# Kernel tuning notes

Measured on AMD Instinct MI355X. Metric: run time of the kernel, lower is better.

The kernel has to match this reference:

```python
import jax, jax.numpy as jnp
import numpy as np

N = 2_000_000
C_IN = 32
C_OUT = 64
K_TAPS = 8  # kernel_size=2 in 3D -> 2^3 taps
EPS = 1e-5


def setup_inputs() -> dict:
    key = jax.random.key(0)
    k1, k2, k3, k4, k5 = jax.random.split(key, 5)
    features = jax.random.normal(k1, (N, C_IN), dtype=jnp.float32)
    gamma = jax.random.uniform(k2, (C_IN,), dtype=jnp.float32)
    beta = jnp.zeros((C_IN,), dtype=jnp.float32)
    weight = jax.random.normal(k3, (K_TAPS, C_IN, C_OUT), dtype=jnp.float32)
    # kernel-map: output segment id and kernel-tap id per input point
    out_index = jax.random.randint(k4, (N,), 0, N, dtype=jnp.int64)
    offset_index = jax.random.randint(k5, (N,), 0, K_TAPS, dtype=jnp.int64)
    return {
        "features": features,
        "gamma": gamma,
        "beta": beta,
        "weight": weight,
        "out_index": out_index,
        "offset_index": offset_index,
    }


def reference(features, gamma, beta, weight, out_index, offset_index):
    # BatchNorm over all active points (training-mode batch stats, biased var)
    mean = jnp.mean(features, axis=0)
    var = jnp.var(features, axis=0)
    x = (features - mean) * jax.lax.rsqrt(var + EPS) * gamma + beta
    # ReLU
    x = jnp.maximum(x, 0.0)
    # Sparse conv, stride == kernel_size: each point hits one output cell via one tap.
    # Loop over the fixed 8 kernel taps; mask, dense matmul, scatter-add.
    out = jnp.zeros((N, C_OUT), dtype=features.dtype)
    for tap in range(K_TAPS):
        xt = jnp.where((offset_index == tap)[:, None], x, 0.0)  # [N, C_in]
        contrib = xt @ weight[tap]  # [N, C_out]
        out = out + jax.ops.segment_sum(contrib, out_index, num_segments=N)
    return out
```

## Files before the change

### kernel.cpp

```cpp
#include <hip/hip_runtime.h>
#include <stdint.h>

#define EPS 1e-5f

typedef __attribute__((ext_vector_type(8))) __bf16 bf16x8;
typedef __attribute__((ext_vector_type(8))) unsigned short ushort8;
typedef __attribute__((ext_vector_type(4))) float f32x4;

__device__ __forceinline__ unsigned short f2bf(float f) {
    union { float f; unsigned u; } c; c.f = f;
    unsigned r = c.u + 0x7fffu + ((c.u >> 16) & 1u);
    return (unsigned short)(r >> 16);
}

__global__ void stats_kernel(const float* __restrict__ f, float* __restrict__ ws, int n) {
    __shared__ float s_sum[32];
    __shared__ float s_sq[32];
    int tid = threadIdx.x;
    if (tid < 32) { s_sum[tid] = 0.f; s_sq[tid] = 0.f; }
    __syncthreads();
    int c = tid & 31;
    int g = tid >> 5;
    float sum = 0.f, sq = 0.f;
    for (int r = blockIdx.x * 8 + g; r < n; r += gridDim.x * 8) {
        float v = f[(size_t)r * 32 + c];
        sum += v; sq += v * v;
    }
    atomicAdd(&s_sum[c], sum);
    atomicAdd(&s_sq[c], sq);
    __syncthreads();
    if (tid < 32) {
        atomicAdd(&ws[tid],      s_sum[tid]);
        atomicAdd(&ws[32 + tid], s_sq[tid]);
    }
}

__global__ void finalize_kernel(const float* __restrict__ gamma, const float* __restrict__ beta,
                                float* __restrict__ ws, int n) {
    int c = threadIdx.x;
    if (c < 32) {
        float inv_n = 1.f / (float)n;
        float mean = ws[c] * inv_n;
        float var  = ws[32 + c] * inv_n - mean * mean;
        float scale = gamma[c] * rsqrtf(var + EPS);
        ws[64 + c] = scale;
        ws[96 + c] = beta[c] - mean * scale;
    }
}

__global__ __launch_bounds__(256, 2) void spconv_kernel(
    const float* __restrict__ feat, const float* __restrict__ weight,
    const int* __restrict__ out_idx, const int* __restrict__ off_idx,
    const float* __restrict__ ws, float* __restrict__ out, int n)
{
    const int lane = threadIdx.x & 63;
    const int m    = lane & 15;
    const int quad = lane >> 4;
    const int wave   = blockIdx.x * (blockDim.x >> 6) + (threadIdx.x >> 6);
    const int nwaves = gridDim.x * (blockDim.x >> 6);

    float scl[8], sft[8];
    #pragma unroll
    for (int j = 0; j < 8; ++j) {
        int k = quad * 8 + j;
        scl[j] = ws[64 + k];
        sft[j] = ws[96 + k];
    }

    ushort8 wf[8][4];
    #pragma unroll
    for (int t = 0; t < 8; ++t) {
        #pragma unroll
        for (int cb = 0; cb < 4; ++cb) {
            ushort8 v;
            #pragma unroll
            for (int j = 0; j < 8; ++j) {
                int k = quad * 8 + j;
                v[j] = f2bf(weight[((size_t)t * 32 + k) * 64 + cb * 16 + m]);
            }
            wf[t][cb] = v;
        }
    }

    const ushort8 zz = {0, 0, 0, 0, 0, 0, 0, 0};
    const int ntiles = (n + 15) >> 4;

    for (int tile = wave; tile < ntiles; tile += nwaves) {
        const int p_base = tile << 4;
        const int p  = p_base + m;
        const int pc = p < n ? p : n - 1;

        const f32x4* fp = (const f32x4*)(feat + (size_t)pc * 32 + quad * 8);
        f32x4 x0 = fp[0];
        f32x4 x1 = fp[1];

        ushort8 af;
        #pragma unroll
        for (int j = 0; j < 4; ++j)
            af[j] = f2bf(fmaxf(x0[j] * scl[j] + sft[j], 0.f));
        #pragma unroll
        for (int j = 0; j < 4; ++j)
            af[4 + j] = f2bf(fmaxf(x1[j] * scl[4 + j] + sft[4 + j], 0.f));

        const int tap = (p < n) ? off_idx[p] : -1;

        f32x4 acc[4];
        #pragma unroll
        for (int cb = 0; cb < 4; ++cb) acc[cb] = (f32x4){0.f, 0.f, 0.f, 0.f};

        #pragma unroll
        for (int t = 0; t < 8; ++t) {
            ushort8 am = (tap == t) ? af : zz;
            bf16x8 a = __builtin_bit_cast(bf16x8, am);
            #pragma unroll
            for (int cb = 0; cb < 4; ++cb) {
                acc[cb] = __builtin_amdgcn_mfma_f32_16x16x32_bf16(
                    a, __builtin_bit_cast(bf16x8, wf[t][cb]), acc[cb], 0, 0, 0);
            }
        }

        int o[4]; bool ok[4];
        #pragma unroll
        for (int i = 0; i < 4; ++i) {
            int pr = p_base + quad * 4 + i;
            ok[i] = pr < n;
            o[i]  = ok[i] ? out_idx[pr] : 0;
        }
        #pragma unroll
        for (int cb = 0; cb < 4; ++cb) {
            #pragma unroll
            for (int i = 0; i < 4; ++i) {
                if (ok[i])
                    atomicAdd(out + (size_t)o[i] * 64 + cb * 16 + m, acc[cb][i]);
            }
        }
    }
}

extern "C" void kernel_launch(void* const* d_in, const int* in_sizes, int n_in,
                              void* d_out, int out_size, void* d_ws, size_t ws_size,
                              hipStream_t stream) {
    const float* features  = (const float*)d_in[0];
    const float* gamma     = (const float*)d_in[1];
    const float* beta      = (const float*)d_in[2];
    const float* weight    = (const float*)d_in[3];
    const int*   out_index = (const int*)d_in[4];
    const int*   off_index = (const int*)d_in[5];
    float* out = (float*)d_out;
    float* ws  = (float*)d_ws;
    const int n = in_sizes[0] / 32;

    hipMemsetAsync(d_out, 0, (size_t)out_size * sizeof(float), stream);
    hipMemsetAsync(d_ws, 0, 64 * sizeof(float), stream);

    stats_kernel<<<2048, 256, 0, stream>>>(features, ws, n);
    finalize_kernel<<<1, 64, 0, stream>>>(gamma, beta, ws, n);
    spconv_kernel<<<1024, 256, 0, stream>>>(features, weight, out_index, off_index,
                                            ws, out, n);
}
```

Baseline: 1.140 ms.

## Bucket points by output row block and accumulate in shared memory

Adds a bucketing pass that groups input points by output row block (128 rows) into a fixed-capacity permutation array. A gather kernel then processes one bucket per block, accumulates contributions with LDS atomics, and writes each output block once. This removes the global float atomics and the output memset. The cost is an extra pass with global atomics on bucket counters, random reads of features, and a full-scan fallback when a bucket overflows its capacity. The old path is kept as a fallback when the workspace is too small.

```diff
diff --git a/kernel.cpp b/kernel.cpp
--- a/kernel.cpp
+++ b/kernel.cpp
@@ -2,6 +2,9 @@
 #include <stdint.h>
 
 #define EPS 1e-5f
+#define BROWS 128
+#define BSHIFT 7
+#define CAP 256
 
 typedef __attribute__((ext_vector_type(8))) __bf16 bf16x8;
 typedef __attribute__((ext_vector_type(8))) unsigned short ushort8;
@@ -48,6 +51,131 @@
     }
 }
 
+__global__ __launch_bounds__(256) void bucket_kernel(const int* __restrict__ out_idx,
+                                                     int* __restrict__ cnt,
+                                                     int* __restrict__ perm, int n) {
+    for (int i = blockIdx.x * blockDim.x + threadIdx.x; i < n;
+         i += gridDim.x * blockDim.x) {
+        int b = out_idx[i] >> BSHIFT;
+        int slot = atomicAdd(&cnt[b], 1);
+        if (slot < CAP) perm[b * CAP + slot] = i;
+    }
+}
+
+__global__ __launch_bounds__(256, 2) void gather_kernel(
+    const float* __restrict__ feat, const float* __restrict__ weight,
+    const int* __restrict__ out_idx, const int* __restrict__ off_idx,
+    const float* __restrict__ ws, const int* __restrict__ cnt,
+    const int* __restrict__ perm, float* __restrict__ out, int n, int nb)
+{
+    __shared__ float s_acc[BROWS][64];
+    const int lane = threadIdx.x & 63;
+    const int m    = lane & 15;
+    const int quad = lane >> 4;
+    const int wid  = threadIdx.x >> 6;
+
+    float scl[8], sft[8];
+    #pragma unroll
+    for (int j = 0; j < 8; ++j) {
+        int k = quad * 8 + j;
+        scl[j] = ws[64 + k];
+        sft[j] = ws[96 + k];
+    }
+
+    ushort8 wf[8][4];
+    #pragma unroll
+    for (int t = 0; t < 8; ++t) {
+        #pragma unroll
+        for (int cb = 0; cb < 4; ++cb) {
+            ushort8 v;
+            #pragma unroll
+            for (int j = 0; j < 8; ++j) {
+                int k = quad * 8 + j;
+                v[j] = f2bf(weight[((size_t)t * 32 + k) * 64 + cb * 16 + m]);
+            }
+            wf[t][cb] = v;
+        }
+    }
+
+    const ushort8 zz = {0, 0, 0, 0, 0, 0, 0, 0};
+
+    for (int b = blockIdx.x; b < nb; b += gridDim.x) {
+        f32x4* pz = (f32x4*)&s_acc[0][0];
+        for (int i = threadIdx.x; i < BROWS * 64 / 4; i += blockDim.x)
+            pz[i] = (f32x4){0.f, 0.f, 0.f, 0.f};
+        __syncthreads();
+
+        const int base_row = b << BSHIFT;
+        const int k = cnt[b];
+        const bool rescan = (k > CAP);
+        const int nch = rescan ? ((n + 15) >> 4) : ((k + 15) >> 4);
+
+        for (int c = wid; c < nch; c += 4) {
+            int slot = c * 16 + m;
+            int p; bool active;
+            if (!rescan) {
+                active = slot < k;
+                p = active ? perm[b * CAP + slot] : 0;
+            } else {
+                p = slot;
+                active = p < n;
+            }
+
+            int row = -1, tap = -1;
+            if (active) {
+                int r = out_idx[p] - base_row;
+                if (r >= 0 && r < BROWS) { row = r; tap = off_idx[p]; }
+            }
+
+            const f32x4* fp = (const f32x4*)(feat + (size_t)(active ? p : 0) * 32 + quad * 8);
+            f32x4 x0 = fp[0];
+            f32x4 x1 = fp[1];
+
+            ushort8 af;
+            #pragma unroll
+            for (int j = 0; j < 4; ++j)
+                af[j] = f2bf(fmaxf(x0[j] * scl[j] + sft[j], 0.f));
+            #pragma unroll
+            for (int j = 0; j < 4; ++j)
+                af[4 + j] = f2bf(fmaxf(x1[j] * scl[4 + j] + sft[4 + j], 0.f));
+
+            f32x4 acc[4];
+            #pragma unroll
+            for (int cb = 0; cb < 4; ++cb) acc[cb] = (f32x4){0.f, 0.f, 0.f, 0.f};
+
+            #pragma unroll
+            for (int t = 0; t < 8; ++t) {
+                ushort8 am = (tap == t) ? af : zz;
+                bf16x8 a = __builtin_bit_cast(bf16x8, am);
+                #pragma unroll
+                for (int cb = 0; cb < 4; ++cb) {
+                    acc[cb] = __builtin_amdgcn_mfma_f32_16x16x32_bf16(
+                        a, __builtin_bit_cast(bf16x8, wf[t][cb]), acc[cb], 0, 0, 0);
+                }
+            }
+
+            #pragma unroll
+            for (int i = 0; i < 4; ++i) {
+                int r = __shfl(row, quad * 4 + i, 64);
+                if (r >= 0) {
+                    #pragma unroll
+                    for (int cb = 0; cb < 4; ++cb)
+                        atomicAdd(&s_acc[r][cb * 16 + m], acc[cb][i]);
+                }
+            }
+        }
+        __syncthreads();
+
+        const int rows = min(BROWS, n - base_row);
+        for (int idx = threadIdx.x; idx < rows * 16; idx += blockDim.x) {
+            int r = idx >> 4, c4 = idx & 15;
+            *((f32x4*)(out + (size_t)(base_row + r) * 64) + c4) =
+                *((f32x4*)&s_acc[r][0] + c4);
+        }
+        __syncthreads();
+    }
+}
+
 __global__ __launch_bounds__(256, 2) void spconv_kernel(
     const float* __restrict__ feat, const float* __restrict__ weight,
     const int* __restrict__ out_idx, const int* __restrict__ off_idx,
@@ -150,11 +278,25 @@
     float* ws  = (float*)d_ws;
     const int n = in_sizes[0] / 32;
 
-    hipMemsetAsync(d_out, 0, (size_t)out_size * sizeof(float), stream);
-    hipMemsetAsync(d_ws, 0, 64 * sizeof(float), stream);
-
-    stats_kernel<<<2048, 256, 0, stream>>>(features, ws, n);
-    finalize_kernel<<<1, 64, 0, stream>>>(gamma, beta, ws, n);
-    spconv_kernel<<<1024, 256, 0, stream>>>(features, weight, out_index, off_index,
-                                            ws, out, n);
-}
+    const int nb = (n + BROWS - 1) >> BSHIFT;
+    const size_t need = (size_t)(128 + nb) * sizeof(int) + (size_t)nb * CAP * sizeof(int);
+
+    if (ws_size >= need) {
+        int* cnt  = (int*)(ws + 128);
+        int* perm = cnt + nb;
+        hipMemsetAsync(d_ws, 0, (size_t)(128 + nb) * sizeof(int), stream);
+        stats_kernel<<<2048, 256, 0, stream>>>(features, ws, n);
+        finalize_kernel<<<1, 64, 0, stream>>>(gamma, beta, ws, n);
+        bucket_kernel<<<2048, 256, 0, stream>>>(out_index, cnt, perm, n);
+        int gblocks = nb < 1280 ? nb : 1280;
+        gather_kernel<<<gblocks, 256, 0, stream>>>(features, weight, out_index, off_index,
+                                                   ws, cnt, perm, out, n, nb);
+    } else {
+        hipMemsetAsync(d_out, 0, (size_t)out_size * sizeof(float), stream);
+        hipMemsetAsync(d_ws, 0, 64 * sizeof(float), stream);
+        stats_kernel<<<2048, 256, 0, stream>>>(features, ws, n);
+        finalize_kernel<<<1, 64, 0, stream>>>(gamma, beta, ws, n);
+        spconv_kernel<<<1024, 256, 0, stream>>>(features, weight, out_index, off_index,
+                                                ws, out, n);
+    }
+}
```

New measurement: 1.618 ms. +41.9%, slower.
